# Kernel optimization log

Hardware: AMD Instinct MI355X
Metric: run time of the kernel (lower is better)

Reference implementation:

```python
import jax, jax.numpy as jnp
import numpy as np

B, S, D, H = 2, 2048, 512, 8
DK = D // H


def setup_inputs() -> dict:
    key = jax.random.key(0)
    ks = jax.random.split(key, 6)
    q = jax.random.normal(ks[0], (B, S, D), dtype=jnp.float32)
    k = jax.random.normal(ks[1], (B, S, D), dtype=jnp.float32)
    v = jax.random.normal(ks[2], (B, S, D), dtype=jnp.float32)
    mask = jax.random.randint(ks[3], (1, 1, S, S), 0, 2, dtype=jnp.int32)
    # nn.Linear weights [out, in]; scaled like torch default init
    Wq = jax.random.normal(ks[4], (D, D), dtype=jnp.float32) / np.sqrt(D)
    Wo = jax.random.normal(ks[5], (D, D), dtype=jnp.float32) / np.sqrt(D)
    return {"q": q, "k": k, "v": v, "mask": mask, "Wq": Wq, "Wo": Wo}


def _split_heads(x):
    # [B,S,D] -> [B,H,S,DK]
    return x.reshape(B, S, H, DK).transpose(0, 2, 1, 3)


def reference(q, k, v, mask, Wq, Wo):
    # NOTE: original module applies Wq to q, k AND v (faithful to source bug)
    query = _split_heads(q @ Wq.T)
    key_ = _split_heads(k @ Wq.T)
    value = _split_heads(v @ Wq.T)
    scores = jnp.einsum("bhqd,bhkd->bhqk", query, key_) / np.sqrt(DK).astype(np.float32)
    # original uses masked_fill_(mask==0, 1e-09) BEFORE softmax (not -inf)
    scores = jnp.where(mask == 0, jnp.float32(1e-9), scores)
    attn = jax.nn.softmax(scores, axis=-1)  # dropout p=0.0 -> identity
    x = jnp.einsum("bhqk,bhkd->bhqd", attn, value)
    x = x.transpose(0, 2, 1, 3).reshape(B, S, D)
    return x @ Wo.T
```

## Files before the change

### kernel.cpp

```cpp
#include <hip/hip_runtime.h>
#include <hip/hip_bf16.h>
#include <stdint.h>

#define S_LEN 2048
#define D_MOD 512
#define N_H   8
#define D_K   64

typedef short v8s __attribute__((ext_vector_type(8)));
typedef short v4s __attribute__((ext_vector_type(4)));
typedef float v4f __attribute__((ext_vector_type(4)));

__device__ __forceinline__ short f2bf(float f) {
  union { float f; unsigned u; } a; a.f = f;
  unsigned u = a.u;
  u += 0x7fffu + ((u >> 16) & 1u);
  return (short)(u >> 16);
}

__device__ __forceinline__ v4f mfma16(v8s a, v8s b, v4f c) {
  return __builtin_amdgcn_mfma_f32_16x16x32_bf16(a, b, c, 0, 0, 0);
}

__global__ __launch_bounds__(256) void maskpack_kernel(
    const int* __restrict__ mask, unsigned long long* __restrict__ mp)
{
  int id = blockIdx.x * 256 + threadIdx.x;
  const int4* m4 = (const int4*)(mask + (size_t)id * 64);
  unsigned long long w = 0ull;
#pragma unroll
  for (int j = 0; j < 16; j++) {
    int4 v = m4[j];
    w |= (unsigned long long)(v.x != 0) << (j * 4 + 0);
    w |= (unsigned long long)(v.y != 0) << (j * 4 + 1);
    w |= (unsigned long long)(v.z != 0) << (j * 4 + 2);
    w |= (unsigned long long)(v.w != 0) << (j * 4 + 3);
  }
  mp[id] = w;
}

__global__ __launch_bounds__(256) void proj_kernel(
    const float* __restrict__ q, const float* __restrict__ k,
    const float* __restrict__ v, const float* __restrict__ Wq,
    short* __restrict__ QP, short* __restrict__ KP, short* __restrict__ VT)
{
  const int z = blockIdx.z;
  const float* __restrict__ A = (z == 0) ? q : ((z == 1) ? k : v);
  const int m0 = blockIdx.x * 64, n0 = blockIdx.y * 64;
  const int tid = threadIdx.x;
  const int wave = tid >> 6, lane = tid & 63;
  const int quad = lane >> 4, l15 = lane & 15;
  const int wm = wave >> 1, wn = wave & 1;
  __shared__ short As[64][72];
  __shared__ short Bs[64][72];
  const int row = tid >> 4, c4 = (tid & 15) << 2;
  v4f acc[2][2];
#pragma unroll
  for (int i = 0; i < 2; i++)
#pragma unroll
    for (int j = 0; j < 2; j++) acc[i][j] = (v4f){0.f, 0.f, 0.f, 0.f};

  float4 a4[4], b4[4];
#pragma unroll
  for (int i = 0; i < 4; i++) {
    int fi = tid + i * 256, r = fi >> 4, c = (fi & 15) << 2;
    a4[i] = *(const float4*)&A[(m0 + r) * 512 + c];
    b4[i] = *(const float4*)&Wq[(n0 + r) * 512 + c];
  }

  for (int kk = 0; kk < 512; kk += 64) {
    __syncthreads();
#pragma unroll
    for (int i = 0; i < 4; i++) {
      int fi = tid + i * 256, r = fi >> 4, c = (fi & 15) << 2;
      v4s ap; ap.x = f2bf(a4[i].x); ap.y = f2bf(a4[i].y); ap.z = f2bf(a4[i].z); ap.w = f2bf(a4[i].w);
      *(v4s*)&As[r][c] = ap;
      v4s bp; bp.x = f2bf(b4[i].x); bp.y = f2bf(b4[i].y); bp.z = f2bf(b4[i].z); bp.w = f2bf(b4[i].w);
      *(v4s*)&Bs[r][c] = bp;
    }
    __syncthreads();
    if (kk + 64 < 512) {
#pragma unroll
      for (int i = 0; i < 4; i++) {
        int fi = tid + i * 256, r = fi >> 4, c = (fi & 15) << 2;
        a4[i] = *(const float4*)&A[(m0 + r) * 512 + kk + 64 + c];
        b4[i] = *(const float4*)&Wq[(n0 + r) * 512 + kk + 64 + c];
      }
    }
#pragma unroll
    for (int ms = 0; ms < 2; ms++)
#pragma unroll
      for (int ns = 0; ns < 2; ns++)
#pragma unroll
        for (int ks = 0; ks < 2; ks++) {
          union { v8s v; v4s h2[2]; } a, bb;
          a.h2[0]  = *(const v4s*)&As[wm * 32 + ms * 16 + l15][ks * 32 + quad * 8];
          a.h2[1]  = *(const v4s*)&As[wm * 32 + ms * 16 + l15][ks * 32 + quad * 8 + 4];
          bb.h2[0] = *(const v4s*)&Bs[wn * 32 + ns * 16 + l15][ks * 32 + quad * 8];
          bb.h2[1] = *(const v4s*)&Bs[wn * 32 + ns * 16 + l15][ks * 32 + quad * 8 + 4];
          acc[ms][ns] = mfma16(a.v, bb.v, acc[ms][ns]);
        }
  }
#pragma unroll
  for (int ms = 0; ms < 2; ms++)
#pragma unroll
    for (int ns = 0; ns < 2; ns++) {
      int mb = m0 + wm * 32 + ms * 16 + quad * 4;
      int n  = n0 + wn * 32 + ns * 16 + l15;
      int bI = mb >> 11, s = mb & 2047, hh = n >> 6, dk = n & 63;
      if (z == 2) {
        v4s pv;
        pv.x = f2bf(acc[ms][ns][0]); pv.y = f2bf(acc[ms][ns][1]);
        pv.z = f2bf(acc[ms][ns][2]); pv.w = f2bf(acc[ms][ns][3]);
        *(v4s*)&VT[((bI * N_H + hh) * D_K + dk) * S_LEN + s] = pv;
      } else {
        short* dst = (z == 0) ? QP : KP;
#pragma unroll
        for (int r = 0; r < 4; r++)
          dst[((bI * N_H + hh) * S_LEN + (s + r)) * D_K + dk] = f2bf(acc[ms][ns][r]);
      }
    }
}

__global__ __launch_bounds__(256) void attn_kernel(
    const short* __restrict__ QP, const short* __restrict__ KP,
    const short* __restrict__ VT, const unsigned long long* __restrict__ mp,
    short* __restrict__ XP)
{
  const int h = blockIdx.y, b = blockIdx.z;
  const int tid = threadIdx.x;
  const int wave = tid >> 6, lane = tid & 63;
  const int quad = lane >> 4, l15 = lane & 15;
  const short* Qh = QP + ((b * N_H + h) * S_LEN) * D_K;
  const short* Kh = KP + ((b * N_H + h) * S_LEN) * D_K;
  const short* Vh = VT + ((b * N_H + h) * D_K) * S_LEN;

  __shared__ short Ks[64][72];
  __shared__ short Vs[64][72];
  __shared__ short Pl[4][16 * 68];

  const int qrow = blockIdx.x * 64 + wave * 16;
  const int srow = tid >> 2;
  const int sc   = (tid & 3) * 8;

  v8s aQ[2];
#pragma unroll
  for (int ks = 0; ks < 2; ks++)
    aQ[ks] = *(const v8s*)&Qh[(qrow + l15) * D_K + ks * 32 + quad * 8];

  const float MASKP = 3.3546263e-4f;
  float lacc[4] = {0.f, 0.f, 0.f, 0.f};
  v4f accX[4];
#pragma unroll
  for (int t = 0; t < 4; t++) accX[t] = (v4f){0.f, 0.f, 0.f, 0.f};

  v8s kreg0 = *(const v8s*)&Kh[srow * D_K + sc];
  v8s kreg1 = *(const v8s*)&Kh[srow * D_K + sc + 32];
  v8s vreg0 = *(const v8s*)&Vh[srow * S_LEN + sc];
  v8s vreg1 = *(const v8s*)&Vh[srow * S_LEN + sc + 32];

  for (int kt = 0; kt < 32; kt++) {
    __syncthreads();
    *(v8s*)&Ks[srow][sc]      = kreg0;
    *(v8s*)&Ks[srow][sc + 32] = kreg1;
    *(v8s*)&Vs[srow][sc]      = vreg0;
    *(v8s*)&Vs[srow][sc + 32] = vreg1;

    unsigned long long mw[4];
#pragma unroll
    for (int r = 0; r < 4; r++) mw[r] = mp[(qrow + quad * 4 + r) * 32 + kt];

    __syncthreads();

    if (kt + 1 < 32) {
      const int c1 = (kt + 1) * 64;
      kreg0 = *(const v8s*)&Kh[(c1 + srow) * D_K + sc];
      kreg1 = *(const v8s*)&Kh[(c1 + srow) * D_K + sc + 32];
      vreg0 = *(const v8s*)&Vh[srow * S_LEN + c1 + sc];
      vreg1 = *(const v8s*)&Vh[srow * S_LEN + c1 + sc + 32];
    }

#pragma unroll
    for (int t = 0; t < 4; t++) {
      v4f s = (v4f){0.f, 0.f, 0.f, 0.f};
#pragma unroll
      for (int ks = 0; ks < 2; ks++) {
        v8s bK = *(const v8s*)&Ks[t * 16 + l15][ks * 32 + quad * 8];
        s = mfma16(aQ[ks], bK, s);
      }
#pragma unroll
      for (int r = 0; r < 4; r++) {
        int bit = (int)((mw[r] >> (t * 16 + l15)) & 1ull);
        float p = bit ? __expf(fmaf(s[r], 0.125f, -8.0f)) : MASKP;
        lacc[r] += p;
        Pl[wave][(quad * 4 + r) * 68 + t * 16 + l15] = f2bf(p);
      }
    }

    union { v8s v; v4s h2[2]; } aP[2];
#pragma unroll
    for (int ks = 0; ks < 2; ks++) {
      aP[ks].h2[0] = *(const v4s*)&Pl[wave][l15 * 68 + ks * 32 + quad * 8];
      aP[ks].h2[1] = *(const v4s*)&Pl[wave][l15 * 68 + ks * 32 + quad * 8 + 4];
    }
#pragma unroll
    for (int t = 0; t < 4; t++)
#pragma unroll
      for (int ks = 0; ks < 2; ks++) {
        v8s bV = *(const v8s*)&Vs[t * 16 + l15][ks * 32 + quad * 8];
        accX[t] = mfma16(aP[ks].v, bV, accX[t]);
      }
  }

  float linv[4];
#pragma unroll
  for (int r = 0; r < 4; r++) {
    float l = lacc[r];
    l += __shfl_xor(l, 1);
    l += __shfl_xor(l, 2);
    l += __shfl_xor(l, 4);
    l += __shfl_xor(l, 8);
    linv[r] = 1.0f / l;
  }
#pragma unroll
  for (int t = 0; t < 4; t++)
#pragma unroll
    for (int r = 0; r < 4; r++) {
      float x = accX[t][r] * linv[r];
      int srw = qrow + quad * 4 + r;
      XP[(b * S_LEN + srw) * D_MOD + h * D_K + t * 16 + l15] = f2bf(x);
    }
}

__global__ __launch_bounds__(256) void outproj_kernel(
    const short* __restrict__ XP, const float* __restrict__ Wo,
    float* __restrict__ out)
{
  const int m0 = blockIdx.x * 64, n0 = blockIdx.y * 64;
  const int tid = threadIdx.x;
  const int wave = tid >> 6, lane = tid & 63;
  const int quad = lane >> 4, l15 = lane & 15;
  const int wm = wave >> 1, wn = wave & 1;
  __shared__ short As[64][72];
  __shared__ short Bs[64][72];
  v4f acc[2][2];
#pragma unroll
  for (int i = 0; i < 2; i++)
#pragma unroll
    for (int j = 0; j < 2; j++) acc[i][j] = (v4f){0.f, 0.f, 0.f, 0.f};

  v4s xa[4]; float4 b4[4];
#pragma unroll
  for (int i = 0; i < 4; i++) {
    int fi = tid + i * 256, r = fi >> 4, c = (fi & 15) << 2;
    xa[i] = *(const v4s*)&XP[(m0 + r) * 512 + c];
    b4[i] = *(const float4*)&Wo[(n0 + r) * 512 + c];
  }

  for (int kk = 0; kk < 512; kk += 64) {
    __syncthreads();
#pragma unroll
    for (int i = 0; i < 4; i++) {
      int fi = tid + i * 256, r = fi >> 4, c = (fi & 15) << 2;
      *(v4s*)&As[r][c] = xa[i];
      v4s bp; bp.x = f2bf(b4[i].x); bp.y = f2bf(b4[i].y); bp.z = f2bf(b4[i].z); bp.w = f2bf(b4[i].w);
      *(v4s*)&Bs[r][c] = bp;
    }
    __syncthreads();
    if (kk + 64 < 512) {
#pragma unroll
      for (int i = 0; i < 4; i++) {
        int fi = tid + i * 256, r = fi >> 4, c = (fi & 15) << 2;
        xa[i] = *(const v4s*)&XP[(m0 + r) * 512 + kk + 64 + c];
        b4[i] = *(const float4*)&Wo[(n0 + r) * 512 + kk + 64 + c];
      }
    }
#pragma unroll
    for (int ms = 0; ms < 2; ms++)
#pragma unroll
      for (int ns = 0; ns < 2; ns++)
#pragma unroll
        for (int ks = 0; ks < 2; ks++) {
          union { v8s v; v4s h2[2]; } a, bb;
          a.h2[0]  = *(const v4s*)&As[wm * 32 + ms * 16 + l15][ks * 32 + quad * 8];
          a.h2[1]  = *(const v4s*)&As[wm * 32 + ms * 16 + l15][ks * 32 + quad * 8 + 4];
          bb.h2[0] = *(const v4s*)&Bs[wn * 32 + ns * 16 + l15][ks * 32 + quad * 8];
          bb.h2[1] = *(const v4s*)&Bs[wn * 32 + ns * 16 + l15][ks * 32 + quad * 8 + 4];
          acc[ms][ns] = mfma16(a.v, bb.v, acc[ms][ns]);
        }
  }
#pragma unroll
  for (int ms = 0; ms < 2; ms++)
#pragma unroll
    for (int ns = 0; ns < 2; ns++) {
      int n = n0 + wn * 32 + ns * 16 + l15;
#pragma unroll
      for (int r = 0; r < 4; r++) {
        int m = m0 + wm * 32 + ms * 16 + quad * 4 + r;
        out[m * 512 + n] = acc[ms][ns][r];
      }
    }
}

extern "C" void kernel_launch(void* const* d_in, const int* in_sizes, int n_in,
                              void* d_out, int out_size, void* d_ws, size_t ws_size,
                              hipStream_t stream) {
  const float* q  = (const float*)d_in[0];
  const float* k  = (const float*)d_in[1];
  const float* v  = (const float*)d_in[2];
  const int* mask = (const int*)d_in[3];
  const float* Wq = (const float*)d_in[4];
  const float* Wo = (const float*)d_in[5];
  float* out = (float*)d_out;
  char* ws = (char*)d_ws;
  short* QP = (short*)(ws);
  short* KP = (short*)(ws + (4u << 20));
  short* VT = (short*)(ws + (8u << 20));
  short* XP = (short*)(ws + (12u << 20));
  unsigned long long* MP = (unsigned long long*)(ws + (16u << 20));

  maskpack_kernel<<<dim3(256), 256, 0, stream>>>(mask, MP);
  proj_kernel<<<dim3(64, 8, 3), 256, 0, stream>>>(q, k, v, Wq, QP, KP, VT);
  attn_kernel<<<dim3(32, N_H, 2), 256, 0, stream>>>(QP, KP, VT, MP, XP);
  outproj_kernel<<<dim3(64, 8, 1), 256, 0, stream>>>(XP, Wo, out);
}
```

Before: 168.0 us.

## Pre-convert inputs to bf16, split attention keys across two wave halves

Adds a conversion kernel that turns q, k, v, Wq and Wo into bf16 once, so the projection GEMMs load bf16 directly with 16-byte vector loads and no longer convert inside the loop. The attention kernel now runs 512 threads per block, and each half of the block processes half of the key sequence. The two partial accumulators are combined through shared memory at the end. The softmax row sum is computed by an MFMA against a ones vector instead of scalar adds, and mask words are prefetched one tile ahead. The cost is an extra kernel launch and a round trip of about 7 MB through global memory, while attention gains more parallelism at the price of a cross-half reduction.

After: 159.7 us. 5.0% less time.

```diff
diff --git a/kernel.cpp b/kernel.cpp
--- a/kernel.cpp
+++ b/kernel.cpp
@@ -20,6 +20,25 @@
 
 __device__ __forceinline__ v4f mfma16(v8s a, v8s b, v4f c) {
   return __builtin_amdgcn_mfma_f32_16x16x32_bf16(a, b, c, 0, 0, 0);
+}
+
+__global__ __launch_bounds__(256) void cvt_kernel(
+    const float* __restrict__ q, const float* __restrict__ k,
+    const float* __restrict__ v, const float* __restrict__ Wq,
+    const float* __restrict__ Wo,
+    short* __restrict__ qb, short* __restrict__ kb, short* __restrict__ vb,
+    short* __restrict__ Wqb, short* __restrict__ Wob)
+{
+  unsigned g = blockIdx.x * 256 + threadIdx.x;
+  const float* src; short* dst; unsigned off;
+  if (g < 524288u)        { src = q;  dst = qb;  off = g; }
+  else if (g < 1048576u)  { src = k;  dst = kb;  off = g - 524288u; }
+  else if (g < 1572864u)  { src = v;  dst = vb;  off = g - 1048576u; }
+  else if (g < 1638400u)  { src = Wq; dst = Wqb; off = g - 1572864u; }
+  else                    { src = Wo; dst = Wob; off = g - 1638400u; }
+  float4 x = ((const float4*)src)[off];
+  v4s p; p.x = f2bf(x.x); p.y = f2bf(x.y); p.z = f2bf(x.z); p.w = f2bf(x.w);
+  ((v4s*)dst)[off] = p;
 }
 
 __global__ __launch_bounds__(256) void maskpack_kernel(
@@ -40,12 +59,12 @@
 }
 
 __global__ __launch_bounds__(256) void proj_kernel(
-    const float* __restrict__ q, const float* __restrict__ k,
-    const float* __restrict__ v, const float* __restrict__ Wq,
+    const short* __restrict__ qb, const short* __restrict__ kb,
+    const short* __restrict__ vb, const short* __restrict__ Wqb,
     short* __restrict__ QP, short* __restrict__ KP, short* __restrict__ VT)
 {
   const int z = blockIdx.z;
-  const float* __restrict__ A = (z == 0) ? q : ((z == 1) ? k : v);
+  const short* __restrict__ A = (z == 0) ? qb : ((z == 1) ? kb : vb);
   const int m0 = blockIdx.x * 64, n0 = blockIdx.y * 64;
   const int tid = threadIdx.x;
   const int wave = tid >> 6, lane = tid & 63;
@@ -53,38 +72,35 @@
   const int wm = wave >> 1, wn = wave & 1;
   __shared__ short As[64][72];
   __shared__ short Bs[64][72];
-  const int row = tid >> 4, c4 = (tid & 15) << 2;
   v4f acc[2][2];
 #pragma unroll
   for (int i = 0; i < 2; i++)
 #pragma unroll
     for (int j = 0; j < 2; j++) acc[i][j] = (v4f){0.f, 0.f, 0.f, 0.f};
 
-  float4 a4[4], b4[4];
-#pragma unroll
-  for (int i = 0; i < 4; i++) {
-    int fi = tid + i * 256, r = fi >> 4, c = (fi & 15) << 2;
-    a4[i] = *(const float4*)&A[(m0 + r) * 512 + c];
-    b4[i] = *(const float4*)&Wq[(n0 + r) * 512 + c];
+  v8s a8[2], b8[2];
+#pragma unroll
+  for (int i = 0; i < 2; i++) {
+    int fi = tid + i * 256, r = fi >> 3, c = (fi & 7) << 3;
+    a8[i] = *(const v8s*)&A[(m0 + r) * 512 + c];
+    b8[i] = *(const v8s*)&Wqb[(n0 + r) * 512 + c];
   }
 
   for (int kk = 0; kk < 512; kk += 64) {
     __syncthreads();
 #pragma unroll
-    for (int i = 0; i < 4; i++) {
-      int fi = tid + i * 256, r = fi >> 4, c = (fi & 15) << 2;
-      v4s ap; ap.x = f2bf(a4[i].x); ap.y = f2bf(a4[i].y); ap.z = f2bf(a4[i].z); ap.w = f2bf(a4[i].w);
-      *(v4s*)&As[r][c] = ap;
-      v4s bp; bp.x = f2bf(b4[i].x); bp.y = f2bf(b4[i].y); bp.z = f2bf(b4[i].z); bp.w = f2bf(b4[i].w);
-      *(v4s*)&Bs[r][c] = bp;
+    for (int i = 0; i < 2; i++) {
+      int fi = tid + i * 256, r = fi >> 3, c = (fi & 7) << 3;
+      *(v8s*)&As[r][c] = a8[i];
+      *(v8s*)&Bs[r][c] = b8[i];
     }
     __syncthreads();
     if (kk + 64 < 512) {
 #pragma unroll
-      for (int i = 0; i < 4; i++) {
-        int fi = tid + i * 256, r = fi >> 4, c = (fi & 15) << 2;
-        a4[i] = *(const float4*)&A[(m0 + r) * 512 + kk + 64 + c];
-        b4[i] = *(const float4*)&Wq[(n0 + r) * 512 + kk + 64 + c];
+      for (int i = 0; i < 2; i++) {
+        int fi = tid + i * 256, r = fi >> 3, c = (fi & 7) << 3;
+        a8[i] = *(const v8s*)&A[(m0 + r) * 512 + kk + 64 + c];
+        b8[i] = *(const v8s*)&Wqb[(n0 + r) * 512 + kk + 64 + c];
       }
     }
 #pragma unroll
@@ -122,26 +138,33 @@
     }
 }
 
-__global__ __launch_bounds__(256) void attn_kernel(
+__global__ __launch_bounds__(512, 4) void attn_kernel(
     const short* __restrict__ QP, const short* __restrict__ KP,
     const short* __restrict__ VT, const unsigned long long* __restrict__ mp,
     short* __restrict__ XP)
 {
   const int h = blockIdx.y, b = blockIdx.z;
   const int tid = threadIdx.x;
-  const int wave = tid >> 6, lane = tid & 63;
+  const int wave = tid >> 6;
+  const int half = wave >> 2;
+  const int wq   = wave & 3;
+  const int lane = tid & 63;
   const int quad = lane >> 4, l15 = lane & 15;
   const short* Qh = QP + ((b * N_H + h) * S_LEN) * D_K;
   const short* Kh = KP + ((b * N_H + h) * S_LEN) * D_K;
   const short* Vh = VT + ((b * N_H + h) * D_K) * S_LEN;
 
-  __shared__ short Ks[64][72];
-  __shared__ short Vs[64][72];
-  __shared__ short Pl[4][16 * 68];
-
-  const int qrow = blockIdx.x * 64 + wave * 16;
-  const int srow = tid >> 2;
-  const int sc   = (tid & 3) * 8;
+  __shared__ char smem[54272];
+  short* Ks = (short*)smem + half * 4608;
+  short* Vs = (short*)(smem + 18432) + half * 4608;
+  short* Pl = (short*)(smem + 36864) + wave * 1088;
+  float* CB = (float*)smem;
+
+  const int qrow = blockIdx.x * 64 + wq * 16;
+  const int t8   = tid & 255;
+  const int srow = t8 >> 2;
+  const int sc   = (t8 & 3) * 8;
+  const int ch0  = half * 1024;
 
   v8s aQ[2];
 #pragma unroll
@@ -149,35 +172,37 @@
     aQ[ks] = *(const v8s*)&Qh[(qrow + l15) * D_K + ks * 32 + quad * 8];
 
   const float MASKP = 3.3546263e-4f;
-  float lacc[4] = {0.f, 0.f, 0.f, 0.f};
-  v4f accX[4];
+  const v8s ONES = {16256,16256,16256,16256,16256,16256,16256,16256};
+  v4f accX[4], accL = (v4f){0.f, 0.f, 0.f, 0.f};
 #pragma unroll
   for (int t = 0; t < 4; t++) accX[t] = (v4f){0.f, 0.f, 0.f, 0.f};
 
-  v8s kreg0 = *(const v8s*)&Kh[srow * D_K + sc];
-  v8s kreg1 = *(const v8s*)&Kh[srow * D_K + sc + 32];
-  v8s vreg0 = *(const v8s*)&Vh[srow * S_LEN + sc];
-  v8s vreg1 = *(const v8s*)&Vh[srow * S_LEN + sc + 32];
-
-  for (int kt = 0; kt < 32; kt++) {
-    __syncthreads();
-    *(v8s*)&Ks[srow][sc]      = kreg0;
-    *(v8s*)&Ks[srow][sc + 32] = kreg1;
-    *(v8s*)&Vs[srow][sc]      = vreg0;
-    *(v8s*)&Vs[srow][sc + 32] = vreg1;
-
-    unsigned long long mw[4];
-#pragma unroll
-    for (int r = 0; r < 4; r++) mw[r] = mp[(qrow + quad * 4 + r) * 32 + kt];
-
-    __syncthreads();
-
-    if (kt + 1 < 32) {
-      const int c1 = (kt + 1) * 64;
+  v8s kreg0 = *(const v8s*)&Kh[(ch0 + srow) * D_K + sc];
+  v8s kreg1 = *(const v8s*)&Kh[(ch0 + srow) * D_K + sc + 32];
+  v8s vreg0 = *(const v8s*)&Vh[srow * S_LEN + ch0 + sc];
+  v8s vreg1 = *(const v8s*)&Vh[srow * S_LEN + ch0 + sc + 32];
+  unsigned long long mwc[4], mwn[4];
+#pragma unroll
+  for (int r = 0; r < 4; r++)
+    mwc[r] = mp[(qrow + quad * 4 + r) * 32 + half * 16];
+
+  for (int kt = 0; kt < 16; kt++) {
+    __syncthreads();
+    *(v8s*)&Ks[srow * 72 + sc]      = kreg0;
+    *(v8s*)&Ks[srow * 72 + sc + 32] = kreg1;
+    *(v8s*)&Vs[srow * 72 + sc]      = vreg0;
+    *(v8s*)&Vs[srow * 72 + sc + 32] = vreg1;
+    __syncthreads();
+
+    if (kt + 1 < 16) {
+      const int c1 = ch0 + (kt + 1) * 64;
       kreg0 = *(const v8s*)&Kh[(c1 + srow) * D_K + sc];
       kreg1 = *(const v8s*)&Kh[(c1 + srow) * D_K + sc + 32];
       vreg0 = *(const v8s*)&Vh[srow * S_LEN + c1 + sc];
       vreg1 = *(const v8s*)&Vh[srow * S_LEN + c1 + sc + 32];
+#pragma unroll
+      for (int r = 0; r < 4; r++)
+        mwn[r] = mp[(qrow + quad * 4 + r) * 32 + half * 16 + kt + 1];
     }
 
 #pragma unroll
@@ -185,55 +210,70 @@
       v4f s = (v4f){0.f, 0.f, 0.f, 0.f};
 #pragma unroll
       for (int ks = 0; ks < 2; ks++) {
-        v8s bK = *(const v8s*)&Ks[t * 16 + l15][ks * 32 + quad * 8];
+        v8s bK = *(const v8s*)&Ks[(t * 16 + l15) * 72 + ks * 32 + quad * 8];
         s = mfma16(aQ[ks], bK, s);
       }
 #pragma unroll
       for (int r = 0; r < 4; r++) {
-        int bit = (int)((mw[r] >> (t * 16 + l15)) & 1ull);
+        int bit = (int)((mwc[r] >> (t * 16 + l15)) & 1ull);
         float p = bit ? __expf(fmaf(s[r], 0.125f, -8.0f)) : MASKP;
-        lacc[r] += p;
-        Pl[wave][(quad * 4 + r) * 68 + t * 16 + l15] = f2bf(p);
+        Pl[(quad * 4 + r) * 68 + t * 16 + l15] = f2bf(p);
       }
     }
 
     union { v8s v; v4s h2[2]; } aP[2];
 #pragma unroll
     for (int ks = 0; ks < 2; ks++) {
-      aP[ks].h2[0] = *(const v4s*)&Pl[wave][l15 * 68 + ks * 32 + quad * 8];
-      aP[ks].h2[1] = *(const v4s*)&Pl[wave][l15 * 68 + ks * 32 + quad * 8 + 4];
+      aP[ks].h2[0] = *(const v4s*)&Pl[l15 * 68 + ks * 32 + quad * 8];
+      aP[ks].h2[1] = *(const v4s*)&Pl[l15 * 68 + ks * 32 + quad * 8 + 4];
     }
 #pragma unroll
     for (int t = 0; t < 4; t++)
 #pragma unroll
       for (int ks = 0; ks < 2; ks++) {
-        v8s bV = *(const v8s*)&Vs[t * 16 + l15][ks * 32 + quad * 8];
+        v8s bV = *(const v8s*)&Vs[(t * 16 + l15) * 72 + ks * 32 + quad * 8];
         accX[t] = mfma16(aP[ks].v, bV, accX[t]);
       }
-  }
-
-  float linv[4];
-#pragma unroll
-  for (int r = 0; r < 4; r++) {
-    float l = lacc[r];
-    l += __shfl_xor(l, 1);
-    l += __shfl_xor(l, 2);
-    l += __shfl_xor(l, 4);
-    l += __shfl_xor(l, 8);
-    linv[r] = 1.0f / l;
-  }
-#pragma unroll
-  for (int t = 0; t < 4; t++)
-#pragma unroll
-    for (int r = 0; r < 4; r++) {
-      float x = accX[t][r] * linv[r];
-      int srw = qrow + quad * 4 + r;
-      XP[(b * S_LEN + srw) * D_MOD + h * D_K + t * 16 + l15] = f2bf(x);
-    }
+    accL = mfma16(aP[0].v, ONES, accL);
+    accL = mfma16(aP[1].v, ONES, accL);
+
+#pragma unroll
+    for (int r = 0; r < 4; r++) mwc[r] = mwn[r];
+  }
+
+  __syncthreads();
+  if (half == 1) {
+    float* c = CB + (wq * 64 + lane) * 21;
+#pragma unroll
+    for (int t = 0; t < 4; t++)
+#pragma unroll
+      for (int r = 0; r < 4; r++) c[t * 4 + r] = accX[t][r];
+#pragma unroll
+    for (int r = 0; r < 4; r++) c[16 + r] = accL[r];
+  }
+  __syncthreads();
+  if (half == 0) {
+    const float* c = CB + (wq * 64 + lane) * 21;
+#pragma unroll
+    for (int t = 0; t < 4; t++)
+#pragma unroll
+      for (int r = 0; r < 4; r++) accX[t][r] += c[t * 4 + r];
+    float linv[4];
+#pragma unroll
+    for (int r = 0; r < 4; r++) linv[r] = 1.0f / (accL[r] + c[16 + r]);
+#pragma unroll
+    for (int t = 0; t < 4; t++)
+#pragma unroll
+      for (int r = 0; r < 4; r++) {
+        float x = accX[t][r] * linv[r];
+        int srw = qrow + quad * 4 + r;
+        XP[(b * S_LEN + srw) * D_MOD + h * D_K + t * 16 + l15] = f2bf(x);
+      }
+  }
 }
 
 __global__ __launch_bounds__(256) void outproj_kernel(
-    const short* __restrict__ XP, const float* __restrict__ Wo,
+    const short* __restrict__ XP, const short* __restrict__ Wob,
     float* __restrict__ out)
 {
   const int m0 = blockIdx.x * 64, n0 = blockIdx.y * 64;
@@ -249,30 +289,29 @@
 #pragma unroll
     for (int j = 0; j < 2; j++) acc[i][j] = (v4f){0.f, 0.f, 0.f, 0.f};
 
-  v4s xa[4]; float4 b4[4];
-#pragma unroll
-  for (int i = 0; i < 4; i++) {
-    int fi = tid + i * 256, r = fi >> 4, c = (fi & 15) << 2;
-    xa[i] = *(const v4s*)&XP[(m0 + r) * 512 + c];
-    b4[i] = *(const float4*)&Wo[(n0 + r) * 512 + c];
+  v8s a8[2], b8[2];
+#pragma unroll
+  for (int i = 0; i < 2; i++) {
+    int fi = tid + i * 256, r = fi >> 3, c = (fi & 7) << 3;
+    a8[i] = *(const v8s*)&XP[(m0 + r) * 512 + c];
+    b8[i] = *(const v8s*)&Wob[(n0 + r) * 512 + c];
   }
 
   for (int kk = 0; kk < 512; kk += 64) {
     __syncthreads();
 #pragma unroll
-    for (int i = 0; i < 4; i++) {
-      int fi = tid + i * 256, r = fi >> 4, c = (fi & 15) << 2;
-      *(v4s*)&As[r][c] = xa[i];
-      v4s bp; bp.x = f2bf(b4[i].x); bp.y = f2bf(b4[i].y); bp.z = f2bf(b4[i].z); bp.w = f2bf(b4[i].w);
-      *(v4s*)&Bs[r][c] = bp;
+    for (int i = 0; i < 2; i++) {
+      int fi = tid + i * 256, r = fi >> 3, c = (fi & 7) << 3;
+      *(v8s*)&As[r][c] = a8[i];
+      *(v8s*)&Bs[r][c] = b8[i];
     }
     __syncthreads();
     if (kk + 64 < 512) {
 #pragma unroll
-      for (int i = 0; i < 4; i++) {
-        int fi = tid + i * 256, r = fi >> 4, c = (fi & 15) << 2;
-        xa[i] = *(const v4s*)&XP[(m0 + r) * 512 + kk + 64 + c];
-        b4[i] = *(const float4*)&Wo[(n0 + r) * 512 + kk + 64 + c];
+      for (int i = 0; i < 2; i++) {
+        int fi = tid + i * 256, r = fi >> 3, c = (fi & 7) << 3;
+        a8[i] = *(const v8s*)&XP[(m0 + r) * 512 + kk + 64 + c];
+        b8[i] = *(const v8s*)&Wob[(n0 + r) * 512 + kk + 64 + c];
       }
     }
 #pragma unroll
@@ -318,9 +357,15 @@
   short* VT = (short*)(ws + (8u << 20));
   short* XP = (short*)(ws + (12u << 20));
   unsigned long long* MP = (unsigned long long*)(ws + (16u << 20));
-
+  short* qb  = (short*)(ws + (17u << 20));
+  short* kb  = (short*)(ws + (21u << 20));
+  short* vb  = (short*)(ws + (25u << 20));
+  short* Wqb = (short*)(ws + (29u << 20));
+  short* Wob = (short*)(ws + (29u << 20) + (512u << 10));
+
+  cvt_kernel<<<dim3(6656), 256, 0, stream>>>(q, k, v, Wq, Wo, qb, kb, vb, Wqb, Wob);
   maskpack_kernel<<<dim3(256), 256, 0, stream>>>(mask, MP);
-  proj_kernel<<<dim3(64, 8, 3), 256, 0, stream>>>(q, k, v, Wq, QP, KP, VT);
-  attn_kernel<<<dim3(32, N_H, 2), 256, 0, stream>>>(QP, KP, VT, MP, XP);
-  outproj_kernel<<<dim3(64, 8, 1), 256, 0, stream>>>(XP, Wo, out);
-}
+  proj_kernel<<<dim3(64, 8, 3), 256, 0, stream>>>(qb, kb, vb, Wqb, QP, KP, VT);
+  attn_kernel<<<dim3(32, N_H, 2), 512, 0, stream>>>(QP, KP, VT, MP, XP);
+  outproj_kernel<<<dim3(64, 8, 1), 256, 0, stream>>>(XP, Wob, out);
+}
```
